# Performance work log

Measured on AMD Instinct MI355X. Metric: run time of the kernel, lower is better.

Reference implementation:

```python
import jax, jax.numpy as jnp
import numpy as np
import math

L, B, S, D, H, FF = 6, 4, 1024, 1024, 16, 4096
HD = D // H
EPS = 1e-5


def _ln(x, g, b):
    m = jnp.mean(x, axis=-1, keepdims=True)
    v = jnp.mean(jnp.square(x - m), axis=-1, keepdims=True)
    return (x - m) / jnp.sqrt(v + EPS) * g + b


def setup_inputs() -> dict:
    key = jax.random.key(0)
    ks = jax.random.split(key, 8)
    std = 0.02
    inp = {
        'x': jax.random.normal(ks[0], (B, S, D), jnp.float32),
        'lengths': jax.random.randint(ks[1], (B,), S // 2, S + 1),
        'rel_bias': jax.random.normal(ks[2], (H, S, S), jnp.float32) * std,
        'ln1_g': jnp.ones((L, D), jnp.float32),
        'ln1_b': jnp.zeros((L, D), jnp.float32),
        'qkv_w': jax.random.normal(ks[3], (L, D, 3 * D), jnp.float32) * std,
        'qkv_b': jnp.zeros((L, 3 * D), jnp.float32),
        'out_w': jax.random.normal(ks[4], (L, D, D), jnp.float32) * std,
        'out_b': jnp.zeros((L, D), jnp.float32),
        'ln2_g': jnp.ones((L, D), jnp.float32),
        'ln2_b': jnp.zeros((L, D), jnp.float32),
        'fc1_w': jax.random.normal(ks[5], (L, D, FF), jnp.float32) * std,
        'fc1_b': jnp.zeros((L, FF), jnp.float32),
        'fc2_w': jax.random.normal(ks[6], (L, FF, D), jnp.float32) * std,
        'fc2_b': jnp.zeros((L, D), jnp.float32),
    }
    return inp


def reference(x, lengths, rel_bias, ln1_g, ln1_b, qkv_w, qkv_b, out_w, out_b,
              ln2_g, ln2_b, fc1_w, fc1_b, fc2_w, fc2_b):
    # causal additive mask [S,S]: -inf above the diagonal (torch.triu diagonal=1)
    ar = jnp.arange(S)
    causal = jnp.where(ar[None, :] > ar[:, None], -jnp.inf, 0.0).astype(x.dtype)
    # key padding mask [B,S]: True where position is padding
    pad = ar[None, :] >= lengths[:, None]
    scale = 1.0 / math.sqrt(HD)

    for i in range(L):
        # --- attention sub-block (pre-LN) ---
        xn = _ln(x, ln1_g[i], ln1_b[i])
        qkv = xn @ qkv_w[i] + qkv_b[i]                      # [B,S,3D]
        q, k, v = jnp.split(qkv, 3, axis=-1)
        q = q.reshape(B, S, H, HD)
        k = k.reshape(B, S, H, HD)
        v = v.reshape(B, S, H, HD)
        scores = jnp.einsum('bqhd,bkhd->bhqk', q, k) * scale  # [B,H,S,S]
        scores = scores + rel_bias[None] + causal[None, None]
        scores = jnp.where(pad[:, None, None, :], -jnp.inf, scores)
        attn = jax.nn.softmax(scores, axis=-1)
        o = jnp.einsum('bhqk,bkhd->bqhd', attn, v).reshape(B, S, D)
        o = o @ out_w[i] + out_b[i]
        o = jnp.where(pad[:, :, None], 0.0, o)
        x = x + o
        # --- feed-forward sub-block (LN inside FF, residual outside) ---
        h = _ln(x, ln2_g[i], ln2_b[i])
        h = jax.nn.gelu(h @ fc1_w[i] + fc1_b[i], approximate=False)
        h = h @ fc2_w[i] + fc2_b[i]
        x = x + h
    return x
```

## Files before the change

### kernel.cpp

```cpp
#include <hip/hip_runtime.h>
#include <cstdint>
#include <cstddef>

constexpr int L_ = 6, B_ = 4, S_ = 1024, D_ = 1024, H_ = 16, FF_ = 4096;
constexpr int D3_ = 3 * D_;
constexpr int HD_ = D_ / H_;

typedef float f32x4 __attribute__((ext_vector_type(4)));
typedef __bf16 bf16x8 __attribute__((ext_vector_type(8)));
typedef unsigned short u16;
typedef u16 u16x4 __attribute__((ext_vector_type(4)));
typedef u16 u16x8 __attribute__((ext_vector_type(8)));

__device__ __forceinline__ u16 f2bf(float f) {
    union { float f; uint32_t u; } v; v.f = f;
    uint32_t r = v.u + 0x7FFFu + ((v.u >> 16) & 1u);
    return (u16)(r >> 16);
}

__device__ __forceinline__ void gload16(const void* g, void* l) {
    __builtin_amdgcn_global_load_lds(
        (const __attribute__((address_space(1))) unsigned int*)g,
        (__attribute__((address_space(3))) unsigned int*)l,
        16, 0, 0);
}

__global__ __launch_bounds__(256) void cvt_layer(
    const float* __restrict__ qw, const float* __restrict__ ow,
    const float* __restrict__ f1w, const float* __restrict__ f2w,
    u16* __restrict__ tq, u16* __restrict__ to,
    u16* __restrict__ t1, u16* __restrict__ t2)
{
    __shared__ float tile[64][65];
    const int bid = blockIdx.x, tid = threadIdx.x;
    const float* W; u16* WT; int K, N, bn, bk;
    if (bid < 768)       { W = qw;  WT = tq; K = 1024; N = 3072; int t = bid;        bn = (t % 48) * 64; bk = (t / 48) * 64; }
    else if (bid < 1024) { W = ow;  WT = to; K = 1024; N = 1024; int t = bid - 768;  bn = (t % 16) * 64; bk = (t / 16) * 64; }
    else if (bid < 2048) { W = f1w; WT = t1; K = 1024; N = 4096; int t = bid - 1024; bn = (t % 64) * 64; bk = (t / 64) * 64; }
    else                 { W = f2w; WT = t2; K = 4096; N = 1024; int t = bid - 2048; bn = (t % 16) * 64; bk = (t / 16) * 64; }
    #pragma unroll
    for (int i = 0; i < 16; ++i) {
        int idx = i * 256 + tid;
        int r = idx >> 6, c = idx & 63;
        tile[r][c] = W[(size_t)(bk + r) * N + bn + c];
    }
    __syncthreads();
    #pragma unroll
    for (int i = 0; i < 16; ++i) {
        int idx = i * 256 + tid;
        int r = idx >> 6, c = idx & 63;
        WT[(size_t)(bn + r) * K + bk + c] = f2bf(tile[c][r]);
    }
}

__global__ __launch_bounds__(256) void vt_transpose(
    const u16* __restrict__ qkv, u16* __restrict__ vt)
{
    __shared__ u16 tile[64][72];
    const int tid = threadIdx.x;
    const int s0 = blockIdx.x * 64, bh = blockIdx.y;
    const int b = bh >> 4, h = bh & 15;
    #pragma unroll
    for (int i = 0; i < 2; ++i) {
        int idx = tid + i * 256;
        int r = idx >> 3, c8 = (idx & 7) * 8;
        u16x8 v = *(const u16x8*)(qkv + ((size_t)(b * S_ + s0 + r)) * D3_ + 2 * D_ + h * 64 + c8);
        #pragma unroll
        for (int j = 0; j < 8; ++j) tile[c8 + j][r] = v[j];
    }
    __syncthreads();
    #pragma unroll
    for (int i = 0; i < 2; ++i) {
        int idx = tid + i * 256;
        int r = idx >> 3, c8 = (idx & 7) * 8;
        u16x8 v;
        #pragma unroll
        for (int j = 0; j < 8; ++j) v[j] = tile[r][c8 + j];
        *(u16x8*)(vt + ((size_t)(bh * 64 + r)) * S_ + s0 + c8) = v;
    }
}

__global__ __launch_bounds__(256) void ln_kernel(
    const float* __restrict__ X, const float* __restrict__ g,
    const float* __restrict__ bp, u16* __restrict__ out)
{
    const int row = blockIdx.x, tid = threadIdx.x;
    const float* xr = X + (size_t)row * D_;
    f32x4 v = *(const f32x4*)(xr + tid * 4);
    float s  = v[0] + v[1] + v[2] + v[3];
    float s2 = v[0]*v[0] + v[1]*v[1] + v[2]*v[2] + v[3]*v[3];
    #pragma unroll
    for (int off = 32; off >= 1; off >>= 1) {
        s  += __shfl_down(s,  off);
        s2 += __shfl_down(s2, off);
    }
    __shared__ float red[8];
    const int lane = tid & 63, wid = tid >> 6;
    if (lane == 0) { red[wid] = s; red[4 + wid] = s2; }
    __syncthreads();
    s  = red[0] + red[1] + red[2] + red[3];
    s2 = red[4] + red[5] + red[6] + red[7];
    float mean = s * (1.f / D_);
    float var  = s2 * (1.f / D_) - mean * mean;
    float rstd = rsqrtf(var + 1e-5f);
    f32x4 gv = *(const f32x4*)(g  + tid * 4);
    f32x4 bv = *(const f32x4*)(bp + tid * 4);
    u16x4 o4;
    #pragma unroll
    for (int r = 0; r < 4; ++r) o4[r] = f2bf((v[r] - mean) * rstd * gv[r] + bv[r]);
    *(u16x4*)(out + (size_t)row * D_ + tid * 4) = o4;
}

template<int MODE>
__global__ __launch_bounds__(512, 2) void gemm8p(
    const u16* __restrict__ A, const u16* __restrict__ BT,
    const float* __restrict__ bias,
    u16* __restrict__ Cb, float* __restrict__ X,
    const int* __restrict__ lengths,
    int M, int N, int K)
{
    __shared__ __align__(16) char lds[4][32768];
    const int tid = threadIdx.x;
    const int lane = tid & 63;
    const int w = tid >> 6;
    const int grp = lane >> 4, l15 = lane & 15;
    const int wm = w >> 2, wn = w & 3;

    const int gx = gridDim.x, gy = gridDim.y;
    const int nwg = gx * gy * gridDim.z;
    int lid = blockIdx.x + gx * (blockIdx.y + gy * blockIdx.z);
    {
        int q = nwg >> 3, r = nwg & 7;
        int xcd = lid & 7, wi = lid >> 3;
        lid = (xcd < r ? xcd * (q + 1) : r * (q + 1) + (xcd - r) * q) + wi;
    }
    const int bx = lid % gx;
    const int byz = lid / gx;
    const int by = byz % gy, bz = byz / gy;

    const int m0 = by * 256, n0 = bx * 256;
    const int Kh = K / gridDim.z;
    const int k0 = bz * Kh;
    const int NT = Kh >> 5;

    const int lrow = lane >> 2;
    const int cchunk = (lane & 3) ^ ((lane >> 3) & 3);
    const u16* gA = A  + (size_t)(m0 + w * 32 + lrow) * K + k0 + cchunk * 8;
    const u16* gB = BT + (size_t)(n0 + w * 32 + lrow) * K + k0 + cchunk * 8;
    const size_t row16 = (size_t)16 * K;
    const int rslot = (grp ^ ((l15 >> 1) & 3)) * 16;

#define STAGE_A(t) do { const u16* p_ = gA + (size_t)(t) * 32;                \
        char* l_ = &lds[(t) & 3][0] + w * 2048;                               \
        gload16(p_, l_); gload16(p_ + row16, l_ + 1024); } while (0)
#define STAGE_B(t) do { const u16* p_ = gB + (size_t)(t) * 32;                \
        char* l_ = &lds[(t) & 3][16384] + w * 2048;                           \
        gload16(p_, l_); gload16(p_ + row16, l_ + 1024); } while (0)

    f32x4 acc[8][4] = {};

    STAGE_A(0); STAGE_B(0);
    STAGE_A(1); STAGE_B(1);
    STAGE_A(2); STAGE_B(2);
    asm volatile("s_waitcnt vmcnt(8)" ::: "memory");
    __builtin_amdgcn_s_barrier();

    for (int t = 0; t < NT; ++t) {
        const char* Ab = &lds[t & 3][0];
        const char* Bb = &lds[t & 3][16384];
        bf16x8 bfr[4], af[4];

        #pragma unroll
        for (int nf = 0; nf < 4; ++nf)
            bfr[nf] = *(const bf16x8*)(Bb + (wn * 64 + nf * 16 + l15) * 64 + rslot);
        #pragma unroll
        for (int mf = 0; mf < 4; ++mf)
            af[mf] = *(const bf16x8*)(Ab + (wm * 128 + mf * 16 + l15) * 64 + rslot);
        if (t + 3 < NT) STAGE_A(t + 3);
        __builtin_amdgcn_s_barrier();
        asm volatile("s_waitcnt lgkmcnt(0)" ::: "memory");
        __builtin_amdgcn_sched_barrier(0);
        __builtin_amdgcn_s_setprio(1);
        #pragma unroll
        for (int mf = 0; mf < 4; ++mf)
            #pragma unroll
            for (int nf = 0; nf < 4; ++nf)
                acc[mf][nf] = __builtin_amdgcn_mfma_f32_16x16x32_bf16(
                    af[mf], bfr[nf], acc[mf][nf], 0, 0, 0);
        __builtin_amdgcn_s_setprio(0);
        __builtin_amdgcn_s_barrier();

        #pragma unroll
        for (int mf = 0; mf < 4; ++mf)
            af[mf] = *(const bf16x8*)(Ab + (wm * 128 + 64 + mf * 16 + l15) * 64 + rslot);
        if (t + 3 < NT) STAGE_B(t + 3);
        if (t + 3 < NT)      asm volatile("s_waitcnt vmcnt(8)" ::: "memory");
        else if (t + 2 < NT) asm volatile("s_waitcnt vmcnt(4)" ::: "memory");
        else                 asm volatile("s_waitcnt vmcnt(0)" ::: "memory");
        __builtin_amdgcn_s_barrier();
        asm volatile("s_waitcnt lgkmcnt(0)" ::: "memory");
        __builtin_amdgcn_sched_barrier(0);
        __builtin_amdgcn_s_setprio(1);
        #pragma unroll
        for (int mf = 0; mf < 4; ++mf)
            #pragma unroll
            for (int nf = 0; nf < 4; ++nf)
                acc[4 + mf][nf] = __builtin_amdgcn_mfma_f32_16x16x32_bf16(
                    af[mf], bfr[nf], acc[4 + mf][nf], 0, 0, 0);
        __builtin_amdgcn_s_setprio(0);
        __builtin_amdgcn_s_barrier();
    }
#undef STAGE_A
#undef STAGE_B

    const float bscale = (k0 == 0) ? 1.f : 0.f;
    #pragma unroll
    for (int mi = 0; mi < 8; ++mi) {
        int row_g = m0 + wm * 128 + mi * 16 + grp * 4;
        #pragma unroll
        for (int nf = 0; nf < 4; ++nf) {
            int col_g = n0 + wn * 64 + nf * 16 + l15;
            float bv = bias[col_g] * bscale;
            f32x4 v = acc[mi][nf];
            if constexpr (MODE == 0) {
                #pragma unroll
                for (int r = 0; r < 4; ++r)
                    Cb[(size_t)(row_g + r) * N + col_g] = f2bf(v[r] + bv);
            } else if constexpr (MODE == 2) {
                #pragma unroll
                for (int r = 0; r < 4; ++r) {
                    float tv = v[r] + bv;
                    float ge = 0.5f * tv * (1.f + erff(tv * 0.70710678118654752f));
                    Cb[(size_t)(row_g + r) * N + col_g] = f2bf(ge);
                }
            } else if constexpr (MODE == 1) {
                int len = lengths[row_g >> 10];
                #pragma unroll
                for (int r = 0; r < 4; ++r) {
                    int row = row_g + r;
                    float add = ((row & 1023) >= len) ? 0.f : (v[r] + bv);
                    atomicAdd(&X[(size_t)row * N + col_g], add);
                }
            } else {
                #pragma unroll
                for (int r = 0; r < 4; ++r)
                    atomicAdd(&X[(size_t)(row_g + r) * N + col_g], v[r] + bv);
            }
        }
    }
}

__global__ __launch_bounds__(256) void attn_kernel(
    const u16* __restrict__ qkv,
    const u16* __restrict__ vt,
    const float* __restrict__ rel_bias,
    const int* __restrict__ lengths,
    u16* __restrict__ obuf)
{
    __shared__ __align__(16) char kls[64 * 128];
    __shared__ __align__(16) char vls[64 * 128];
    const int tid = threadIdx.x, lane = tid & 63, wid = tid >> 6;
    const int grp = lane >> 4, l15 = lane & 15;
    const int qt = blockIdx.x, bh = blockIdx.y;
    const int b = bh >> 4, h = bh & 15;
    const int len = lengths[b];
    const int qrow = qt * 64 + wid * 16 + l15;

    bf16x8 qf[2];
    {
        const u16* qp = qkv + ((size_t)(b * S_ + qrow)) * D3_ + h * 64 + grp * 8;
        qf[0] = *(const bf16x8*)qp;
        qf[1] = *(const bf16x8*)(qp + 32);
    }
    f32x4 oacc[4] = {};
    float m_run = -INFINITY, lsum = 0.f;
    int kt_end = (len + 63) >> 6;
    if (qt + 1 < kt_end) kt_end = qt + 1;

    for (int kt = 0; kt < kt_end; ++kt) {
        __syncthreads();
        #pragma unroll
        for (int i = 0; i < 2; ++i) {
            int id2 = tid + i * 256;
            int r = id2 >> 3, gg = id2 & 7;
            int sw = (r & 7) << 4;
            bf16x8 kv = *(const bf16x8*)(qkv + ((size_t)(b * S_ + kt * 64 + r)) * D3_ + D_ + h * 64 + gg * 8);
            *(bf16x8*)(kls + r * 128 + ((gg * 16) ^ sw)) = kv;
            bf16x8 vv = *(const bf16x8*)(vt + ((size_t)(bh * 64 + r)) * S_ + kt * 64 + gg * 8);
            *(bf16x8*)(vls + r * 128 + ((gg * 16) ^ sw)) = vv;
        }
        __syncthreads();

        f32x4 sf[4] = {};
        #pragma unroll
        for (int f = 0; f < 4; ++f) {
            int r = f * 16 + l15;
            int sw = (r & 7) << 4;
            #pragma unroll
            for (int t = 0; t < 2; ++t) {
                bf16x8 af = *(const bf16x8*)(kls + r * 128 + (((t * 32 + grp * 8) * 2) ^ sw));
                sf[f] = __builtin_amdgcn_mfma_f32_16x16x32_bf16(af, qf[t], sf[f], 0, 0, 0);
            }
        }
        float p[4][4];
        float tmax = -INFINITY;
        #pragma unroll
        for (int f = 0; f < 4; ++f) {
            f32x4 bi = *(const f32x4*)(rel_bias + ((size_t)h * S_ + qrow) * S_ + kt * 64 + f * 16 + grp * 4);
            #pragma unroll
            for (int r = 0; r < 4; ++r) {
                int kp = kt * 64 + f * 16 + grp * 4 + r;
                bool valid = (kp <= qrow) && (kp < len);
                float sv = valid ? fmaf(sf[f][r], 0.125f, bi[r]) : -INFINITY;
                p[f][r] = sv;
                tmax = fmaxf(tmax, sv);
            }
        }
        tmax = fmaxf(tmax, __shfl_xor(tmax, 16));
        tmax = fmaxf(tmax, __shfl_xor(tmax, 32));
        float m_new = fmaxf(m_run, tmax);
        float alpha = expf(m_run - m_new);
        float psum = 0.f;
        #pragma unroll
        for (int f = 0; f < 4; ++f)
            #pragma unroll
            for (int r = 0; r < 4; ++r) {
                float e = expf(p[f][r] - m_new);
                p[f][r] = e; psum += e;
            }
        psum += __shfl_xor(psum, 16);
        psum += __shfl_xor(psum, 32);
        lsum = lsum * alpha + psum;
        m_run = m_new;
        #pragma unroll
        for (int fo = 0; fo < 4; ++fo) {
            oacc[fo][0] *= alpha; oacc[fo][1] *= alpha;
            oacc[fo][2] *= alpha; oacc[fo][3] *= alpha;
        }
        #pragma unroll
        for (int t = 0; t < 2; ++t) {
            union { u16 u[8]; bf16x8 v; } pb;
            #pragma unroll
            for (int j = 0; j < 4; ++j) {
                pb.u[j]     = f2bf(p[2 * t][j]);
                pb.u[4 + j] = f2bf(p[2 * t + 1][j]);
            }
            #pragma unroll
            for (int fo = 0; fo < 4; ++fo) {
                int r = fo * 16 + l15;
                int sw = (r & 7) << 4;
                union { u16x4 h4[2]; bf16x8 v; } av;
                av.h4[0] = *(const u16x4*)(vls + r * 128 + ((t * 64 + grp * 8)      ^ sw));
                av.h4[1] = *(const u16x4*)(vls + r * 128 + ((t * 64 + grp * 8 + 32) ^ sw));
                oacc[fo] = __builtin_amdgcn_mfma_f32_16x16x32_bf16(av.v, pb.v, oacc[fo], 0, 0, 0);
            }
        }
    }
    float inv = 1.f / lsum;
    #pragma unroll
    for (int fo = 0; fo < 4; ++fo)
        #pragma unroll
        for (int r = 0; r < 4; ++r) {
            int hd = fo * 16 + grp * 4 + r;
            obuf[((size_t)(b * S_) + qrow) * D_ + h * 64 + hd] = f2bf(oacc[fo][r] * inv);
        }
}

extern "C" void kernel_launch(void* const* d_in, const int* in_sizes, int n_in,
                              void* d_out, int out_size, void* d_ws, size_t ws_size,
                              hipStream_t stream)
{
    const float* x_in     = (const float*)d_in[0];
    const int*   lengths  = (const int*)d_in[1];
    const float* rel_bias = (const float*)d_in[2];
    const float* ln1_g    = (const float*)d_in[3];
    const float* ln1_b    = (const float*)d_in[4];
    const float* qkv_w    = (const float*)d_in[5];
    const float* qkv_b    = (const float*)d_in[6];
    const float* out_w    = (const float*)d_in[7];
    const float* out_b    = (const float*)d_in[8];
    const float* ln2_g    = (const float*)d_in[9];
    const float* ln2_b    = (const float*)d_in[10];
    const float* fc1_w    = (const float*)d_in[11];
    const float* fc1_b    = (const float*)d_in[12];
    const float* fc2_w    = (const float*)d_in[13];
    const float* fc2_b    = (const float*)d_in[14];
    float* X = (float*)d_out;

    char* ws = (char*)d_ws;
    size_t off = 0;
    auto alloc = [&](size_t bytes) {
        char* p = ws + off;
        off = (off + bytes + 255) & ~(size_t)255;
        return p;
    };
    u16* wT_qkv = (u16*)alloc((size_t)D3_ * D_ * 2);
    u16* wT_out = (u16*)alloc((size_t)D_ * D_ * 2);
    u16* wT_fc1 = (u16*)alloc((size_t)FF_ * D_ * 2);
    u16* wT_fc2 = (u16*)alloc((size_t)D_ * FF_ * 2);
    u16* xn     = (u16*)alloc((size_t)B_ * S_ * D_ * 2);
    u16* qkvb   = (u16*)alloc((size_t)B_ * S_ * D3_ * 2);
    u16* vtb    = (u16*)alloc((size_t)B_ * H_ * HD_ * S_ * 2);
    u16* ob     = (u16*)alloc((size_t)B_ * S_ * D_ * 2);
    u16* h1     = (u16*)alloc((size_t)B_ * S_ * FF_ * 2);

    const int M = B_ * S_;

    hipMemcpyAsync(X, x_in, (size_t)M * D_ * sizeof(float),
                   hipMemcpyDeviceToDevice, stream);

    for (int i = 0; i < L_; ++i) {
        cvt_layer<<<3072, 256, 0, stream>>>(
            qkv_w + (size_t)i * D_ * D3_, out_w + (size_t)i * D_ * D_,
            fc1_w + (size_t)i * D_ * FF_, fc2_w + (size_t)i * FF_ * D_,
            wT_qkv, wT_out, wT_fc1, wT_fc2);

        ln_kernel<<<M, 256, 0, stream>>>(X, ln1_g + i * D_, ln1_b + i * D_, xn);
        gemm8p<0><<<dim3(D3_ / 256, M / 256, 1), 512, 0, stream>>>(
            xn, wT_qkv, qkv_b + (size_t)i * D3_, qkvb, nullptr, nullptr, M, D3_, D_);
        vt_transpose<<<dim3(S_ / 64, B_ * H_), 256, 0, stream>>>(qkvb, vtb);
        attn_kernel<<<dim3(S_ / 64, B_ * H_), 256, 0, stream>>>(
            qkvb, vtb, rel_bias, lengths, ob);
        gemm8p<1><<<dim3(D_ / 256, M / 256, 4), 512, 0, stream>>>(
            ob, wT_out, out_b + (size_t)i * D_, nullptr, X, lengths, M, D_, D_);

        ln_kernel<<<M, 256, 0, stream>>>(X, ln2_g + i * D_, ln2_b + i * D_, xn);
        gemm8p<2><<<dim3(FF_ / 256, M / 256, 1), 512, 0, stream>>>(
            xn, wT_fc1, fc1_b + (size_t)i * FF_, h1, nullptr, nullptr, M, FF_, D_);
        gemm8p<3><<<dim3(D_ / 256, M / 256, 4), 512, 0, stream>>>(
            h1, wT_fc2, fc2_b + (size_t)i * D_, nullptr, X, nullptr, M, D_, FF_);
    }
}
```

Before: 1.936 ms.

## Fuse V-transpose into QKV GEMM, bf16 rel_bias, retile GEMM to 256x128

The QKV GEMM epilogue now writes V straight into the transposed layout, which removes the separate vt_transpose kernel. rel_bias is converted once to bf16 so the attention kernel reads half the bytes. The GEMM moves from 512-thread 256x256 tiles to 256-thread 256x128 tiles with a simpler triple-buffered pipeline, and the attention grid order is swapped. The trade-offs are bf16 precision loss on the bias, scattered 8-byte stores for V^T, and a different GEMM occupancy and pipelining balance.

Measured after the change: 1.962 ms. No clear change (+1.3%).

```diff
diff --git a/kernel.cpp b/kernel.cpp
--- a/kernel.cpp
+++ b/kernel.cpp
@@ -17,12 +17,28 @@
     uint32_t r = v.u + 0x7FFFu + ((v.u >> 16) & 1u);
     return (u16)(r >> 16);
 }
+__device__ __forceinline__ float bf2f(u16 u) {
+    union { uint32_t u; float f; } v; v.u = ((uint32_t)u) << 16;
+    return v.f;
+}
 
 __device__ __forceinline__ void gload16(const void* g, void* l) {
     __builtin_amdgcn_global_load_lds(
         (const __attribute__((address_space(1))) unsigned int*)g,
         (__attribute__((address_space(3))) unsigned int*)l,
         16, 0, 0);
+}
+
+__global__ __launch_bounds__(256) void cvt_bias(
+    const float* __restrict__ src, u16* __restrict__ dst)
+{
+    size_t i = ((size_t)blockIdx.x * 256 + threadIdx.x) * 8;
+    f32x4 a = *(const f32x4*)(src + i);
+    f32x4 b = *(const f32x4*)(src + i + 4);
+    u16x8 o;
+    #pragma unroll
+    for (int r = 0; r < 4; ++r) { o[r] = f2bf(a[r]); o[4 + r] = f2bf(b[r]); }
+    *(u16x8*)(dst + i) = o;
 }
 
 __global__ __launch_bounds__(256) void cvt_layer(
@@ -50,33 +66,6 @@
         int idx = i * 256 + tid;
         int r = idx >> 6, c = idx & 63;
         WT[(size_t)(bn + r) * K + bk + c] = f2bf(tile[c][r]);
-    }
-}
-
-__global__ __launch_bounds__(256) void vt_transpose(
-    const u16* __restrict__ qkv, u16* __restrict__ vt)
-{
-    __shared__ u16 tile[64][72];
-    const int tid = threadIdx.x;
-    const int s0 = blockIdx.x * 64, bh = blockIdx.y;
-    const int b = bh >> 4, h = bh & 15;
-    #pragma unroll
-    for (int i = 0; i < 2; ++i) {
-        int idx = tid + i * 256;
-        int r = idx >> 3, c8 = (idx & 7) * 8;
-        u16x8 v = *(const u16x8*)(qkv + ((size_t)(b * S_ + s0 + r)) * D3_ + 2 * D_ + h * 64 + c8);
-        #pragma unroll
-        for (int j = 0; j < 8; ++j) tile[c8 + j][r] = v[j];
-    }
-    __syncthreads();
-    #pragma unroll
-    for (int i = 0; i < 2; ++i) {
-        int idx = tid + i * 256;
-        int r = idx >> 3, c8 = (idx & 7) * 8;
-        u16x8 v;
-        #pragma unroll
-        for (int j = 0; j < 8; ++j) v[j] = tile[r][c8 + j];
-        *(u16x8*)(vt + ((size_t)(bh * 64 + r)) * S_ + s0 + c8) = v;
     }
 }
 
@@ -112,19 +101,22 @@
 }
 
 template<int MODE>
-__global__ __launch_bounds__(512, 2) void gemm8p(
+__global__ __launch_bounds__(256, 2) void gemmk(
     const u16* __restrict__ A, const u16* __restrict__ BT,
     const float* __restrict__ bias,
-    u16* __restrict__ Cb, float* __restrict__ X,
+    u16* __restrict__ Cb, float* __restrict__ X, u16* __restrict__ VT,
     const int* __restrict__ lengths,
     int M, int N, int K)
 {
-    __shared__ __align__(16) char lds[4][32768];
+    __shared__ __align__(16) char sb0[24576];
+    __shared__ __align__(16) char sb1[24576];
+    __shared__ __align__(16) char sb2[24576];
+
     const int tid = threadIdx.x;
     const int lane = tid & 63;
     const int w = tid >> 6;
     const int grp = lane >> 4, l15 = lane & 15;
-    const int wm = w >> 2, wn = w & 3;
+    const int wm = w >> 1, wn = w & 1;
 
     const int gx = gridDim.x, gy = gridDim.y;
     const int nwg = gx * gy * gridDim.z;
@@ -138,80 +130,63 @@
     const int byz = lid / gx;
     const int by = byz % gy, bz = byz / gy;
 
-    const int m0 = by * 256, n0 = bx * 256;
+    const int m0 = by * 256, n0 = bx * 128;
     const int Kh = K / gridDim.z;
     const int k0 = bz * Kh;
     const int NT = Kh >> 5;
 
     const int lrow = lane >> 2;
     const int cchunk = (lane & 3) ^ ((lane >> 3) & 3);
-    const u16* gA = A  + (size_t)(m0 + w * 32 + lrow) * K + k0 + cchunk * 8;
+    const u16* gA = A  + (size_t)(m0 + w * 64 + lrow) * K + k0 + cchunk * 8;
     const u16* gB = BT + (size_t)(n0 + w * 32 + lrow) * K + k0 + cchunk * 8;
     const size_t row16 = (size_t)16 * K;
     const int rslot = (grp ^ ((l15 >> 1) & 3)) * 16;
 
-#define STAGE_A(t) do { const u16* p_ = gA + (size_t)(t) * 32;                \
-        char* l_ = &lds[(t) & 3][0] + w * 2048;                               \
-        gload16(p_, l_); gload16(p_ + row16, l_ + 1024); } while (0)
-#define STAGE_B(t) do { const u16* p_ = gB + (size_t)(t) * 32;                \
-        char* l_ = &lds[(t) & 3][16384] + w * 2048;                           \
-        gload16(p_, l_); gload16(p_ + row16, l_ + 1024); } while (0)
+#define STAGE(t, BUF) do {                                                    \
+        const u16* pa_ = gA + (size_t)(t) * 32;                               \
+        const u16* pb_ = gB + (size_t)(t) * 32;                               \
+        char* la_ = (BUF) + w * 4096;                                         \
+        char* lb_ = (BUF) + 16384 + w * 2048;                                 \
+        gload16(pa_,              la_);                                       \
+        gload16(pa_ + row16,      la_ + 1024);                                \
+        gload16(pa_ + 2 * row16,  la_ + 2048);                                \
+        gload16(pa_ + 3 * row16,  la_ + 3072);                                \
+        gload16(pb_,              lb_);                                       \
+        gload16(pb_ + row16,      lb_ + 1024); } while (0)
 
     f32x4 acc[8][4] = {};
 
-    STAGE_A(0); STAGE_B(0);
-    STAGE_A(1); STAGE_B(1);
-    STAGE_A(2); STAGE_B(2);
-    asm volatile("s_waitcnt vmcnt(8)" ::: "memory");
-    __builtin_amdgcn_s_barrier();
+    STAGE(0, sb0);
+    if (NT > 1) STAGE(1, sb1);
+    char* bA = sb0; char* bB = sb1; char* bC = sb2;
 
     for (int t = 0; t < NT; ++t) {
-        const char* Ab = &lds[t & 3][0];
-        const char* Bb = &lds[t & 3][16384];
-        bf16x8 bfr[4], af[4];
-
+        if (t + 1 < NT) asm volatile("s_waitcnt vmcnt(6)" ::: "memory");
+        else            asm volatile("s_waitcnt vmcnt(0)" ::: "memory");
+        __builtin_amdgcn_s_barrier();
+        if (t + 2 < NT) STAGE(t + 2, bC);
+
+        const char* Ab = bA;
+        const char* Bb = bA + 16384;
+        bf16x8 bfr[4], af[8];
         #pragma unroll
         for (int nf = 0; nf < 4; ++nf)
             bfr[nf] = *(const bf16x8*)(Bb + (wn * 64 + nf * 16 + l15) * 64 + rslot);
         #pragma unroll
-        for (int mf = 0; mf < 4; ++mf)
+        for (int mf = 0; mf < 8; ++mf)
             af[mf] = *(const bf16x8*)(Ab + (wm * 128 + mf * 16 + l15) * 64 + rslot);
-        if (t + 3 < NT) STAGE_A(t + 3);
-        __builtin_amdgcn_s_barrier();
-        asm volatile("s_waitcnt lgkmcnt(0)" ::: "memory");
-        __builtin_amdgcn_sched_barrier(0);
         __builtin_amdgcn_s_setprio(1);
         #pragma unroll
-        for (int mf = 0; mf < 4; ++mf)
+        for (int mf = 0; mf < 8; ++mf)
             #pragma unroll
             for (int nf = 0; nf < 4; ++nf)
                 acc[mf][nf] = __builtin_amdgcn_mfma_f32_16x16x32_bf16(
                     af[mf], bfr[nf], acc[mf][nf], 0, 0, 0);
         __builtin_amdgcn_s_setprio(0);
-        __builtin_amdgcn_s_barrier();
-
-        #pragma unroll
-        for (int mf = 0; mf < 4; ++mf)
-            af[mf] = *(const bf16x8*)(Ab + (wm * 128 + 64 + mf * 16 + l15) * 64 + rslot);
-        if (t + 3 < NT) STAGE_B(t + 3);
-        if (t + 3 < NT)      asm volatile("s_waitcnt vmcnt(8)" ::: "memory");
-        else if (t + 2 < NT) asm volatile("s_waitcnt vmcnt(4)" ::: "memory");
-        else                 asm volatile("s_waitcnt vmcnt(0)" ::: "memory");
-        __builtin_amdgcn_s_barrier();
-        asm volatile("s_waitcnt lgkmcnt(0)" ::: "memory");
-        __builtin_amdgcn_sched_barrier(0);
-        __builtin_amdgcn_s_setprio(1);
-        #pragma unroll
-        for (int mf = 0; mf < 4; ++mf)
-            #pragma unroll
-            for (int nf = 0; nf < 4; ++nf)
-                acc[4 + mf][nf] = __builtin_amdgcn_mfma_f32_16x16x32_bf16(
-                    af[mf], bfr[nf], acc[4 + mf][nf], 0, 0, 0);
-        __builtin_amdgcn_s_setprio(0);
-        __builtin_amdgcn_s_barrier();
-    }
-#undef STAGE_A
-#undef STAGE_B
+
+        char* tmp = bA; bA = bB; bB = bC; bC = tmp;
+    }
+#undef STAGE
 
     const float bscale = (k0 == 0) ? 1.f : 0.f;
     #pragma unroll
@@ -223,9 +198,17 @@
             float bv = bias[col_g] * bscale;
             f32x4 v = acc[mi][nf];
             if constexpr (MODE == 0) {
-                #pragma unroll
-                for (int r = 0; r < 4; ++r)
-                    Cb[(size_t)(row_g + r) * N + col_g] = f2bf(v[r] + bv);
+                if (col_g < 2 * D_) {
+                    #pragma unroll
+                    for (int r = 0; r < 4; ++r)
+                        Cb[(size_t)(row_g + r) * N + col_g] = f2bf(v[r] + bv);
+                } else {
+                    u16x4 o4;
+                    #pragma unroll
+                    for (int r = 0; r < 4; ++r) o4[r] = f2bf(v[r] + bv);
+                    int vrow = ((row_g >> 10) << 10) + (col_g - 2 * D_);
+                    *(u16x4*)(VT + (size_t)vrow * S_ + (row_g & 1023)) = o4;
+                }
             } else if constexpr (MODE == 2) {
                 #pragma unroll
                 for (int r = 0; r < 4; ++r) {
@@ -253,7 +236,7 @@
 __global__ __launch_bounds__(256) void attn_kernel(
     const u16* __restrict__ qkv,
     const u16* __restrict__ vt,
-    const float* __restrict__ rel_bias,
+    const u16* __restrict__ rbb,
     const int* __restrict__ lengths,
     u16* __restrict__ obuf)
 {
@@ -261,7 +244,7 @@
     __shared__ __align__(16) char vls[64 * 128];
     const int tid = threadIdx.x, lane = tid & 63, wid = tid >> 6;
     const int grp = lane >> 4, l15 = lane & 15;
-    const int qt = blockIdx.x, bh = blockIdx.y;
+    const int bh = blockIdx.x, qt = blockIdx.y;
     const int b = bh >> 4, h = bh & 15;
     const int len = lengths[b];
     const int qrow = qt * 64 + wid * 16 + l15;
@@ -306,12 +289,12 @@
         float tmax = -INFINITY;
         #pragma unroll
         for (int f = 0; f < 4; ++f) {
-            f32x4 bi = *(const f32x4*)(rel_bias + ((size_t)h * S_ + qrow) * S_ + kt * 64 + f * 16 + grp * 4);
+            u16x4 bi = *(const u16x4*)(rbb + ((size_t)h * S_ + qrow) * S_ + kt * 64 + f * 16 + grp * 4);
             #pragma unroll
             for (int r = 0; r < 4; ++r) {
                 int kp = kt * 64 + f * 16 + grp * 4 + r;
                 bool valid = (kp <= qrow) && (kp < len);
-                float sv = valid ? fmaf(sf[f][r], 0.125f, bi[r]) : -INFINITY;
+                float sv = valid ? fmaf(sf[f][r], 0.125f, bf2f(bi[r])) : -INFINITY;
                 p[f][r] = sv;
                 tmax = fmaxf(tmax, sv);
             }
@@ -403,11 +386,13 @@
     u16* vtb    = (u16*)alloc((size_t)B_ * H_ * HD_ * S_ * 2);
     u16* ob     = (u16*)alloc((size_t)B_ * S_ * D_ * 2);
     u16* h1     = (u16*)alloc((size_t)B_ * S_ * FF_ * 2);
+    u16* rbb    = (u16*)alloc((size_t)H_ * S_ * S_ * 2);
 
     const int M = B_ * S_;
 
     hipMemcpyAsync(X, x_in, (size_t)M * D_ * sizeof(float),
                    hipMemcpyDeviceToDevice, stream);
+    cvt_bias<<<(H_ * S_ * S_) / (256 * 8), 256, 0, stream>>>(rel_bias, rbb);
 
     for (int i = 0; i < L_; ++i) {
         cvt_layer<<<3072, 256, 0, stream>>>(
@@ -416,18 +401,17 @@
             wT_qkv, wT_out, wT_fc1, wT_fc2);
 
         ln_kernel<<<M, 256, 0, stream>>>(X, ln1_g + i * D_, ln1_b + i * D_, xn);
-        gemm8p<0><<<dim3(D3_ / 256, M / 256, 1), 512, 0, stream>>>(
-            xn, wT_qkv, qkv_b + (size_t)i * D3_, qkvb, nullptr, nullptr, M, D3_, D_);
-        vt_transpose<<<dim3(S_ / 64, B_ * H_), 256, 0, stream>>>(qkvb, vtb);
-        attn_kernel<<<dim3(S_ / 64, B_ * H_), 256, 0, stream>>>(
-            qkvb, vtb, rel_bias, lengths, ob);
-        gemm8p<1><<<dim3(D_ / 256, M / 256, 4), 512, 0, stream>>>(
-            ob, wT_out, out_b + (size_t)i * D_, nullptr, X, lengths, M, D_, D_);
+        gemmk<0><<<dim3(D3_ / 128, M / 256, 1), 256, 0, stream>>>(
+            xn, wT_qkv, qkv_b + (size_t)i * D3_, qkvb, nullptr, vtb, nullptr, M, D3_, D_);
+        attn_kernel<<<dim3(B_ * H_, S_ / 64), 256, 0, stream>>>(
+            qkvb, vtb, rbb, lengths, ob);
+        gemmk<1><<<dim3(D_ / 128, M / 256, 4), 256, 0, stream>>>(
+            ob, wT_out, out_b + (size_t)i * D_, nullptr, X, nullptr, lengths, M, D_, D_);
 
         ln_kernel<<<M, 256, 0, stream>>>(X, ln2_g + i * D_, ln2_b + i * D_, xn);
-        gemm8p<2><<<dim3(FF_ / 256, M / 256, 1), 512, 0, stream>>>(
-            xn, wT_fc1, fc1_b + (size_t)i * FF_, h1, nullptr, nullptr, M, FF_, D_);
-        gemm8p<3><<<dim3(D_ / 256, M / 256, 4), 512, 0, stream>>>(
-            h1, wT_fc2, fc2_b + (size_t)i * D_, nullptr, X, nullptr, M, D_, FF_);
-    }
-}
+        gemmk<2><<<dim3(FF_ / 128, M / 256, 1), 256, 0, stream>>>(
+            xn, wT_fc1, fc1_b + (size_t)i * FF_, h1, nullptr, nullptr, nullptr, M, FF_, D_);
+        gemmk<3><<<dim3(D_ / 128, M / 256, 4), 256, 0, stream>>>(
+            h1, wT_fc2, fc2_b + (size_t)i * D_, nullptr, X, nullptr, nullptr, M, D_, FF_);
+    }
+}
```
